# Optimization experiments

Hardware: AMD Instinct MI355X
Metric: run time of the kernel (lower is better)

Reference implementation:

```python
import jax, jax.numpy as jnp
import numpy as np

B, C, H, W = 8, 512, 32, 32
NUM_HEADS, D_K = 8, 64
EPS = 1e-5


def setup_inputs() -> dict:
    key = jax.random.key(0)
    ks = jax.random.split(key, 6)
    s = 1.0 / np.sqrt(C)
    return {
        "x": jax.random.normal(ks[0], (B, C, H, W), dtype=jnp.float32),
        "wq": jax.random.uniform(ks[1], (C, NUM_HEADS * D_K), jnp.float32, -s, s),
        "bq": jnp.zeros((NUM_HEADS * D_K,), jnp.float32),
        "wk": jax.random.uniform(ks[2], (C, NUM_HEADS * D_K), jnp.float32, -s, s),
        "bk": jnp.zeros((NUM_HEADS * D_K,), jnp.float32),
        "wv": jax.random.uniform(ks[3], (C, NUM_HEADS * D_K), jnp.float32, -s, s),
        "bv": jnp.zeros((NUM_HEADS * D_K,), jnp.float32),
        "ln_g": jnp.ones((C,), jnp.float32),
        "ln_b": jnp.zeros((C,), jnp.float32),
        "wo": jax.random.uniform(ks[4], (NUM_HEADS * D_K, C), jnp.float32, -s, s),
        "bo": jnp.zeros((C,), jnp.float32),
    }


def reference(x, wq, bq, wk, bk, wv, bv, ln_g, ln_b, wo, bo):
    b, c, h, w = x.shape
    seq = h * w
    # [B, C, H, W] -> [B, S, C]
    t = x.reshape(b, c, seq).transpose(0, 2, 1)
    residual = t
    # LayerNorm over channel dim
    mu = jnp.mean(t, axis=-1, keepdims=True)
    var = jnp.var(t, axis=-1, keepdims=True)
    tn = (t - mu) * jax.lax.rsqrt(var + EPS) * ln_g + ln_b
    # QKV projections -> [B, S, h, d]
    q = (tn @ wq + bq).reshape(b, seq, NUM_HEADS, D_K)
    k = (tn @ wk + bk).reshape(b, seq, NUM_HEADS, D_K)
    v = (tn @ wv + bv).reshape(b, seq, NUM_HEADS, D_K)
    scores = jnp.einsum("bqhd,bkhd->bhqk", q, k) / np.sqrt(D_K).astype(np.float32)
    attn = jax.nn.softmax(scores, axis=-1)
    out = jnp.einsum("bhqk,bkhd->bqhd", attn, v).reshape(b, seq, NUM_HEADS * D_K)
    out = out @ wo + bo
    return out + residual
```

## Files before the change

kernel.cpp:

```cpp
#include <hip/hip_runtime.h>
#include <hip/hip_bf16.h>
#include <stdint.h>

#define BB 8
#define CC 512
#define SS 1024
#define NH 8
#define DK 64
#define MM (BB*SS)
#define PQ 72

typedef __attribute__((ext_vector_type(8))) short bf16x8;
typedef __attribute__((ext_vector_type(4))) float f32x4;

__device__ inline float b2f(unsigned short u) {
    union { unsigned int i; float f; } x; x.i = ((unsigned int)u) << 16; return x.f;
}
__device__ inline unsigned short f2b(float f) {
    union { float f; unsigned int i; } x; x.f = f;
    unsigned int r = (x.i + 0x7FFFu + ((x.i >> 16) & 1u)) >> 16;
    return (unsigned short)r;
}
__device__ inline unsigned int cvtpk(float lo, float hi) {
    unsigned int r;
    asm("v_cvt_pk_bf16_f32 %0, %1, %2" : "=v"(r) : "v"(lo), "v"(hi));
    return r;
}
__device__ inline f32x4 mfma16(bf16x8 a, bf16x8 b, f32x4 c) {
    return __builtin_amdgcn_mfma_f32_16x16x32_bf16(a, b, c, 0, 0, 0);
}
__device__ __forceinline__ void gload16(const void* g, void* l) {
    __builtin_amdgcn_global_load_lds(
        (const __attribute__((address_space(1))) void*)g,
        (__attribute__((address_space(3))) void*)l, 16, 0, 0);
}

__global__ void __launch_bounds__(256) wtrans_kernel(const float* __restrict__ wq,
                                                     const float* __restrict__ wk,
                                                     const float* __restrict__ wv,
                                                     const float* __restrict__ wo,
                                                     unsigned short* __restrict__ wT) {
    __shared__ float lds[64][65];
    const float* w = (blockIdx.z == 0) ? wq : (blockIdx.z == 1) ? wk : (blockIdx.z == 2) ? wv : wo;
    unsigned short* o = wT + (size_t)blockIdx.z * (512 * 512);
    const int n0 = blockIdx.x * 64, k0 = blockIdx.y * 64;
    const int t = threadIdx.x;
    {
        const int nl = (t & 15) * 4, kr = t >> 4;
#pragma unroll
        for (int i = 0; i < 4; ++i) {
            float4 v = *(const float4*)(w + (size_t)(k0 + kr + i * 16) * 512 + n0 + nl);
            lds[kr + i * 16][nl] = v.x; lds[kr + i * 16][nl + 1] = v.y;
            lds[kr + i * 16][nl + 2] = v.z; lds[kr + i * 16][nl + 3] = v.w;
        }
    }
    __syncthreads();
    {
        const int k8 = (t & 7) * 8, nr = t >> 3;
#pragma unroll
        for (int ii = 0; ii < 2; ++ii) {
            int n = nr + ii * 32;
            unsigned short pk[8];
#pragma unroll
            for (int e = 0; e < 8; ++e) pk[e] = f2b(lds[k8 + e][n]);
            *(uint4*)&o[(size_t)(n0 + n) * 512 + k0 + k8] = *(uint4*)pk;
        }
    }
}

__global__ void __launch_bounds__(256) stats_kernel(const float* __restrict__ x,
                                                    float2* __restrict__ stats) {
    __shared__ float2 red[16][64];
    const int b = blockIdx.y, s0 = blockIdx.x * 64;
    const int sl = (threadIdx.x & 15) * 4, cg = threadIdx.x >> 4;
    float sum[4] = {0.f, 0.f, 0.f, 0.f}, sq[4] = {0.f, 0.f, 0.f, 0.f};
    const float* xp = x + ((size_t)b * 512 + cg * 32) * 1024 + s0 + sl;
#pragma unroll 4
    for (int i = 0; i < 32; ++i) {
        float4 v = *(const float4*)(xp + (size_t)i * 1024);
        sum[0] += v.x; sq[0] += v.x * v.x;
        sum[1] += v.y; sq[1] += v.y * v.y;
        sum[2] += v.z; sq[2] += v.z * v.z;
        sum[3] += v.w; sq[3] += v.w * v.w;
    }
#pragma unroll
    for (int e = 0; e < 4; ++e) red[cg][sl + e] = make_float2(sum[e], sq[e]);
    __syncthreads();
    if (threadIdx.x < 64) {
        float s = 0.f, q = 0.f;
#pragma unroll
        for (int c = 0; c < 16; ++c) { s += red[c][threadIdx.x].x; q += red[c][threadIdx.x].y; }
        float mean = s * (1.f / 512.f);
        float var = q * (1.f / 512.f) - mean * mean;
        stats[b * 1024 + s0 + threadIdx.x] = make_float2(mean, rsqrtf(var + 1e-5f));
    }
}

__global__ void __launch_bounds__(256) xln_kernel(const float* __restrict__ x,
                                                  const float2* __restrict__ stats,
                                                  const float* __restrict__ g,
                                                  const float* __restrict__ bta,
                                                  unsigned short* __restrict__ xt,
                                                  unsigned short* __restrict__ tn) {
    __shared__ float lds[64][65];
    const int s0 = blockIdx.x * 64, c0 = blockIdx.y * 64, b = blockIdx.z;
    const int t = threadIdx.x;
    {
        const int sl = (t & 15) * 4, cr = t >> 4;
#pragma unroll
        for (int i = 0; i < 4; ++i) {
            float4 v = *(const float4*)(x + ((size_t)b * 512 + c0 + cr + i * 16) * 1024 + s0 + sl);
            lds[cr + i * 16][sl] = v.x; lds[cr + i * 16][sl + 1] = v.y;
            lds[cr + i * 16][sl + 2] = v.z; lds[cr + i * 16][sl + 3] = v.w;
        }
    }
    __syncthreads();
    {
        const int c8 = (t & 7) * 8, sr = t >> 3;
        float gg[8], bb[8];
        {
            float4 g0 = *(const float4*)(g + c0 + c8), g1 = *(const float4*)(g + c0 + c8 + 4);
            float4 b0 = *(const float4*)(bta + c0 + c8), b1 = *(const float4*)(bta + c0 + c8 + 4);
            gg[0]=g0.x; gg[1]=g0.y; gg[2]=g0.z; gg[3]=g0.w; gg[4]=g1.x; gg[5]=g1.y; gg[6]=g1.z; gg[7]=g1.w;
            bb[0]=b0.x; bb[1]=b0.y; bb[2]=b0.z; bb[3]=b0.w; bb[4]=b1.x; bb[5]=b1.y; bb[6]=b1.z; bb[7]=b1.w;
        }
#pragma unroll
        for (int ii = 0; ii < 2; ++ii) {
            int s = sr + ii * 32;
            float2 st = stats[b * 1024 + s0 + s];
            unsigned short rawp[8], nrmp[8];
#pragma unroll
            for (int e = 0; e < 8; ++e) {
                float v = lds[c8 + e][s];
                rawp[e] = f2b(v);
                nrmp[e] = f2b((v - st.x) * st.y * gg[e] + bb[e]);
            }
            *(uint4*)&xt[((size_t)b * 1024 + s0 + s) * 512 + c0 + c8] = *(uint4*)rawp;
            *(uint4*)&tn[((size_t)b * 1024 + s0 + s) * 512 + c0 + c8] = *(uint4*)nrmp;
        }
    }
}

__device__ inline void gemm_tile(const unsigned short* __restrict__ A,
                                 const unsigned short* __restrict__ Bt,
                                 int m0, int n0,
                                 unsigned short (*A_lds)[128 * 64],
                                 unsigned short (*B_lds)[128 * 64],
                                 f32x4 acc[4][4]) {
    const int t = threadIdx.x;
    const int lane = t & 63, w = t >> 6;
    const int l15 = lane & 15, l4 = lane >> 4;
    const int wm = (w >> 1) * 64, wn = (w & 1) * 64;
    auto STAGE = [&](int bi, int kt) {
#pragma unroll
        for (int i = 0; i < 4; ++i) {
            int chunk = i * 256 + t;
            int row = chunk >> 3, kc = (chunk & 7) * 8;
            gload16(A + (size_t)(m0 + row) * 512 + kt * 64 + kc, &A_lds[bi][chunk * 8]);
            gload16(Bt + (size_t)(n0 + row) * 512 + kt * 64 + kc, &B_lds[bi][chunk * 8]);
        }
    };
    STAGE(0, 0);
    __syncthreads();
#pragma unroll 1
    for (int kt = 0; kt < 8; ++kt) {
        const int bi = kt & 1;
        if (kt < 7) STAGE(bi ^ 1, kt + 1);
#pragma unroll
        for (int kk = 0; kk < 2; ++kk) {
            bf16x8 af[4], bfr[4];
#pragma unroll
            for (int i = 0; i < 4; ++i)
                af[i] = *(const bf16x8*)&A_lds[bi][(wm + i * 16 + l15) * 64 + kk * 32 + l4 * 8];
#pragma unroll
            for (int j = 0; j < 4; ++j)
                bfr[j] = *(const bf16x8*)&B_lds[bi][(wn + j * 16 + l15) * 64 + kk * 32 + l4 * 8];
#pragma unroll
            for (int i = 0; i < 4; ++i)
#pragma unroll
                for (int j = 0; j < 4; ++j)
                    acc[i][j] = mfma16(af[i], bfr[j], acc[i][j]);
        }
        __syncthreads();
    }
}

__global__ void __launch_bounds__(256) gemm_qkv_kernel(const unsigned short* __restrict__ tn,
                                                       const unsigned short* __restrict__ wT,
                                                       const float* __restrict__ bq,
                                                       const float* __restrict__ bk,
                                                       const float* __restrict__ bv,
                                                       unsigned short* __restrict__ outbase) {
    __shared__ alignas(16) unsigned short A_lds[2][128 * 64];
    __shared__ alignas(16) unsigned short B_lds[2][128 * 64];
    const int z = blockIdx.z;
    const unsigned short* Bt = wT + (size_t)z * (512 * 512);
    const float* bias = (z == 0) ? bq : (z == 1) ? bk : bv;
    const int m0 = blockIdx.x * 128, n0 = blockIdx.y * 128;
    f32x4 acc[4][4];
    const f32x4 z4 = {0.f, 0.f, 0.f, 0.f};
#pragma unroll
    for (int i = 0; i < 4; ++i)
#pragma unroll
        for (int j = 0; j < 4; ++j) acc[i][j] = z4;
    gemm_tile(tn, Bt, m0, n0, A_lds, B_lds, acc);
    const int lane = threadIdx.x & 63, w = threadIdx.x >> 6;
    const int l15 = lane & 15, l4 = lane >> 4;
    const int wm = (w >> 1) * 64, wn = (w & 1) * 64;
    if (z < 2) {
        unsigned short* out = outbase + (size_t)z * MM * 512;
#pragma unroll
        for (int i = 0; i < 4; ++i)
#pragma unroll
            for (int j = 0; j < 4; ++j) {
                int col = n0 + wn + j * 16 + l15;
                float bcol = bias[col];
#pragma unroll
                for (int r = 0; r < 4; ++r) {
                    int row = m0 + wm + i * 16 + l4 * 4 + r;
                    out[(size_t)row * 512 + col] = f2b(acc[i][j][r] + bcol);
                }
            }
    } else {
        unsigned short* vt = outbase + (size_t)2 * MM * 512;
#pragma unroll
        for (int i = 0; i < 4; ++i)
#pragma unroll
            for (int j = 0; j < 4; ++j) {
                int col = n0 + wn + j * 16 + l15;
                float bcol = bias[col];
                int rowb = m0 + wm + i * 16 + l4 * 4;
                int bi = rowb >> 10, s0 = rowb & 1023;
                uint2 pk;
                pk.x = (unsigned int)f2b(acc[i][j][0] + bcol) |
                       ((unsigned int)f2b(acc[i][j][1] + bcol) << 16);
                pk.y = (unsigned int)f2b(acc[i][j][2] + bcol) |
                       ((unsigned int)f2b(acc[i][j][3] + bcol) << 16);
                *(uint2*)&vt[((size_t)bi * 512 + col) * 1024 + s0] = pk;
            }
    }
}

__global__ void __launch_bounds__(512) attn_kernel(const unsigned short* __restrict__ q,
                                                   const unsigned short* __restrict__ k,
                                                   const unsigned short* __restrict__ vt,
                                                   unsigned short* __restrict__ o) {
    __shared__ alignas(16) unsigned short Kl[2][64 * 64];
    __shared__ alignas(16) unsigned short Vl[2][64 * 64];
    __shared__ alignas(16) unsigned short Pl[8][16 * PQ];
    const int pid = blockIdx.x;
    const int g = (pid >> 6) * 8 + (pid & 7);
    const int qt = (pid >> 3) & 7;
    const int b = g >> 3, h = g & 7;
    const int t = threadIdx.x, lane = t & 63, w = t >> 6;
    const int l15 = lane & 15, l4 = lane >> 4;

    const float QSC = 0.125f * 1.44269504f;
    const int qrow = qt * 128 + w * 16 + l15;
    const unsigned short* qp = q + ((size_t)(b * SS + qrow)) * 512 + h * 64;
    bf16x8 qf[2];
#pragma unroll
    for (int kk = 0; kk < 2; ++kk) {
        bf16x8 tmp = *(const bf16x8*)(qp + kk * 32 + l4 * 8);
#pragma unroll
        for (int e = 0; e < 8; ++e)
            tmp[e] = (short)f2b(b2f((unsigned short)tmp[e]) * QSC);
        qf[kk] = tmp;
    }

    const int srow = t >> 3;
    const int scb = ((t & 7) * 16) ^ ((srow & 7) << 4);
    const char* kptr = (const char*)(k + ((size_t)(b * SS) + srow) * 512 + h * 64) + scb;
    const char* vptr = (const char*)(vt + ((size_t)(b * NH + h) * DK + srow) * SS) + scb;

    float m_run = -1e30f, l_run = 0.f;
    f32x4 acc_o[4];
    const f32x4 z4 = {0.f, 0.f, 0.f, 0.f};
#pragma unroll
    for (int j = 0; j < 4; ++j) acc_o[j] = z4;

    gload16(kptr, &Kl[0][t * 8]);
    gload16(vptr, &Vl[0][t * 8]);
    kptr += 64 * 512 * 2;
    vptr += 64 * 2;
    __syncthreads();

#pragma unroll 1
    for (int kt = 0; kt < 16; ++kt) {
        const int bi = kt & 1;
        if (kt < 15) {
            gload16(kptr, &Kl[bi ^ 1][t * 8]);
            gload16(vptr, &Vl[bi ^ 1][t * 8]);
            kptr += 64 * 512 * 2;
            vptr += 64 * 2;
        }

        f32x4 sc[4];
#pragma unroll
        for (int j = 0; j < 4; ++j) sc[j] = z4;
#pragma unroll
        for (int kk = 0; kk < 2; ++kk)
#pragma unroll
            for (int j = 0; j < 4; ++j) {
                int row = j * 16 + l15;
                int cb = (kk * 64 + l4 * 16) ^ ((row & 7) << 4);
                bf16x8 kf = *(const bf16x8*)((const char*)Kl[bi] + row * 128 + cb);
                sc[j] = mfma16(kf, qf[kk], sc[j]);
            }

        float mx = fmaxf(fmaxf(sc[0][0], sc[0][1]), fmaxf(sc[0][2], sc[0][3]));
#pragma unroll
        for (int j = 1; j < 4; ++j)
            mx = fmaxf(mx, fmaxf(fmaxf(sc[j][0], sc[j][1]), fmaxf(sc[j][2], sc[j][3])));
        mx = fmaxf(mx, __shfl_xor(mx, 16));
        mx = fmaxf(mx, __shfl_xor(mx, 32));
        const float mnew = fmaxf(m_run, mx);
        const float scl = exp2f(m_run - mnew);
        m_run = mnew;

        float p[4][4], lsum = 0.f;
#pragma unroll
        for (int j = 0; j < 4; ++j)
#pragma unroll
            for (int r = 0; r < 4; ++r) {
                p[j][r] = exp2f(sc[j][r] - mnew);
                lsum += p[j][r];
            }
        l_run = l_run * scl + lsum;

#pragma unroll
        for (int j = 0; j < 4; ++j) {
            uint2 pk;
            pk.x = cvtpk(p[j][0], p[j][1]);
            pk.y = cvtpk(p[j][2], p[j][3]);
            *(uint2*)&Pl[w][l15 * PQ + j * 16 + l4 * 4] = pk;
        }

        float scl_r[4];
#pragma unroll
        for (int r = 0; r < 4; ++r) scl_r[r] = __shfl(scl, (l4 << 2) | r);
#pragma unroll
        for (int j = 0; j < 4; ++j)
#pragma unroll
            for (int r = 0; r < 4; ++r) acc_o[j][r] *= scl_r[r];

#pragma unroll
        for (int kk = 0; kk < 2; ++kk) {
            bf16x8 pf = *(const bf16x8*)&Pl[w][l15 * PQ + kk * 32 + l4 * 8];
#pragma unroll
            for (int j = 0; j < 4; ++j) {
                int row = j * 16 + l15;
                int cb = (kk * 64 + l4 * 16) ^ ((row & 7) << 4);
                bf16x8 vf = *(const bf16x8*)((const char*)Vl[bi] + row * 128 + cb);
                acc_o[j] = mfma16(pf, vf, acc_o[j]);
            }
        }

        __syncthreads();
    }

    float l_tot = l_run;
    l_tot += __shfl_xor(l_tot, 16);
    l_tot += __shfl_xor(l_tot, 32);
    float l_r[4];
#pragma unroll
    for (int r = 0; r < 4; ++r) l_r[r] = __shfl(l_tot, (l4 << 2) | r);

#pragma unroll
    for (int j = 0; j < 4; ++j)
#pragma unroll
        for (int r = 0; r < 4; ++r) {
            int row = qt * 128 + w * 16 + l4 * 4 + r;
            float val = acc_o[j][r] / l_r[r];
            o[((size_t)(b * SS + row)) * 512 + h * 64 + j * 16 + l15] = f2b(val);
        }
}

__global__ void __launch_bounds__(256) gemm_out_kernel(const unsigned short* __restrict__ ao,
                                                       const unsigned short* __restrict__ woT,
                                                       const float* __restrict__ bo,
                                                       const unsigned short* __restrict__ xt,
                                                       float* __restrict__ out) {
    __shared__ alignas(16) unsigned short A_lds[2][128 * 64];
    __shared__ alignas(16) unsigned short B_lds[2][128 * 64];
    const int m0 = blockIdx.x * 128, n0 = blockIdx.y * 128;
    f32x4 acc[4][4];
    const f32x4 z4 = {0.f, 0.f, 0.f, 0.f};
#pragma unroll
    for (int i = 0; i < 4; ++i)
#pragma unroll
        for (int j = 0; j < 4; ++j) acc[i][j] = z4;
    gemm_tile(ao, woT, m0, n0, A_lds, B_lds, acc);
    const int lane = threadIdx.x & 63, w = threadIdx.x >> 6;
    const int l15 = lane & 15, l4 = lane >> 4;
    const int wm = (w >> 1) * 64, wn = (w & 1) * 64;
#pragma unroll
    for (int i = 0; i < 4; ++i)
#pragma unroll
        for (int j = 0; j < 4; ++j) {
            int col = n0 + wn + j * 16 + l15;
            float bcol = bo[col];
#pragma unroll
            for (int r = 0; r < 4; ++r) {
                int row = m0 + wm + i * 16 + l4 * 4 + r;
                float resid = b2f(xt[(size_t)row * 512 + col]);
                out[(size_t)row * 512 + col] = acc[i][j][r] + bcol + resid;
            }
        }
}

extern "C" void kernel_launch(void* const* d_in, const int* in_sizes, int n_in,
                              void* d_out, int out_size, void* d_ws, size_t ws_size,
                              hipStream_t stream) {
    const float* x   = (const float*)d_in[0];
    const float* wq  = (const float*)d_in[1];
    const float* bq  = (const float*)d_in[2];
    const float* wk  = (const float*)d_in[3];
    const float* bk  = (const float*)d_in[4];
    const float* wv  = (const float*)d_in[5];
    const float* bv  = (const float*)d_in[6];
    const float* lng = (const float*)d_in[7];
    const float* lnb = (const float*)d_in[8];
    const float* wo  = (const float*)d_in[9];
    const float* bo  = (const float*)d_in[10];
    float* out = (float*)d_out;

    unsigned short* ws  = (unsigned short*)d_ws;
    const size_t M1 = (size_t)1024 * 1024;
    unsigned short* tn   = ws;
    unsigned short* qkvb = ws + 4 * M1;
    unsigned short* wT   = ws + 16 * M1;
    unsigned short* xt   = ws + 17 * M1;
    unsigned short* ao   = tn;
    float2* stats = (float2*)qkvb;

    wtrans_kernel<<<dim3(8, 8, 4), 256, 0, stream>>>(wq, wk, wv, wo, wT);
    stats_kernel<<<dim3(16, 8), 256, 0, stream>>>(x, stats);
    xln_kernel<<<dim3(16, 8, 8), 256, 0, stream>>>(x, stats, lng, lnb, xt, tn);
    gemm_qkv_kernel<<<dim3(64, 4, 3), 256, 0, stream>>>(tn, wT, bq, bk, bv, qkvb);
    attn_kernel<<<512, 512, 0, stream>>>(qkvb,
                                         qkvb + (size_t)MM * 512,
                                         qkvb + (size_t)2 * MM * 512,
                                         ao);
    gemm_out_kernel<<<dim3(64, 4), 256, 0, stream>>>(ao, wT + (size_t)3 * 512 * 512, bo, xt, out);
}
```

Baseline: 176.4 us.

## Fuse LayerNorm stats into transpose kernel and vectorize GEMM epilogues via swapped MFMA

```diff
diff --git a/kernel.cpp b/kernel.cpp
--- a/kernel.cpp
+++ b/kernel.cpp
@@ -9,6 +9,7 @@
 #define DK 64
 #define MM (BB*SS)
 #define PQ 72
+#define LNP 40
 
 typedef __attribute__((ext_vector_type(8))) short bf16x8;
 typedef __attribute__((ext_vector_type(4))) float f32x4;
@@ -68,79 +69,71 @@
     }
 }
 
-__global__ void __launch_bounds__(256) stats_kernel(const float* __restrict__ x,
-                                                    float2* __restrict__ stats) {
-    __shared__ float2 red[16][64];
-    const int b = blockIdx.y, s0 = blockIdx.x * 64;
-    const int sl = (threadIdx.x & 15) * 4, cg = threadIdx.x >> 4;
+__global__ void __launch_bounds__(256) xlnf_kernel(const float* __restrict__ x,
+                                                   const float* __restrict__ g,
+                                                   const float* __restrict__ bta,
+                                                   unsigned short* __restrict__ xt,
+                                                   unsigned short* __restrict__ tn) {
+    __shared__ unsigned short raw[512 * LNP];
+    __shared__ float2 red[32][33];
+    __shared__ float2 stf[32];
+    const int b = blockIdx.y, s0 = blockIdx.x * 32;
+    const int t = threadIdx.x;
+    const int sl4 = (t & 7) * 4, crow = t >> 3;
     float sum[4] = {0.f, 0.f, 0.f, 0.f}, sq[4] = {0.f, 0.f, 0.f, 0.f};
-    const float* xp = x + ((size_t)b * 512 + cg * 32) * 1024 + s0 + sl;
-#pragma unroll 4
-    for (int i = 0; i < 32; ++i) {
-        float4 v = *(const float4*)(xp + (size_t)i * 1024);
+#pragma unroll
+    for (int ci = 0; ci < 16; ++ci) {
+        const int c = crow + 32 * ci;
+        float4 v = *(const float4*)(x + ((size_t)b * 512 + c) * 1024 + s0 + sl4);
         sum[0] += v.x; sq[0] += v.x * v.x;
         sum[1] += v.y; sq[1] += v.y * v.y;
         sum[2] += v.z; sq[2] += v.z * v.z;
         sum[3] += v.w; sq[3] += v.w * v.w;
-    }
-#pragma unroll
-    for (int e = 0; e < 4; ++e) red[cg][sl + e] = make_float2(sum[e], sq[e]);
+        const int swz = ((c >> 6) & 3) << 3;
+        uint2 pk;
+        pk.x = (unsigned int)f2b(v.x) | ((unsigned int)f2b(v.y) << 16);
+        pk.y = (unsigned int)f2b(v.z) | ((unsigned int)f2b(v.w) << 16);
+        *(uint2*)&raw[c * LNP + (sl4 ^ swz)] = pk;
+    }
+#pragma unroll
+    for (int e = 0; e < 4; ++e) red[crow][sl4 + e] = make_float2(sum[e], sq[e]);
     __syncthreads();
-    if (threadIdx.x < 64) {
+    if (t < 32) {
         float s = 0.f, q = 0.f;
 #pragma unroll
-        for (int c = 0; c < 16; ++c) { s += red[c][threadIdx.x].x; q += red[c][threadIdx.x].y; }
+        for (int cg = 0; cg < 32; ++cg) { s += red[cg][t].x; q += red[cg][t].y; }
         float mean = s * (1.f / 512.f);
         float var = q * (1.f / 512.f) - mean * mean;
-        stats[b * 1024 + s0 + threadIdx.x] = make_float2(mean, rsqrtf(var + 1e-5f));
-    }
-}
-
-__global__ void __launch_bounds__(256) xln_kernel(const float* __restrict__ x,
-                                                  const float2* __restrict__ stats,
-                                                  const float* __restrict__ g,
-                                                  const float* __restrict__ bta,
-                                                  unsigned short* __restrict__ xt,
-                                                  unsigned short* __restrict__ tn) {
-    __shared__ float lds[64][65];
-    const int s0 = blockIdx.x * 64, c0 = blockIdx.y * 64, b = blockIdx.z;
-    const int t = threadIdx.x;
-    {
-        const int sl = (t & 15) * 4, cr = t >> 4;
-#pragma unroll
-        for (int i = 0; i < 4; ++i) {
-            float4 v = *(const float4*)(x + ((size_t)b * 512 + c0 + cr + i * 16) * 1024 + s0 + sl);
-            lds[cr + i * 16][sl] = v.x; lds[cr + i * 16][sl + 1] = v.y;
-            lds[cr + i * 16][sl + 2] = v.z; lds[cr + i * 16][sl + 3] = v.w;
-        }
+        stf[t] = make_float2(mean, rsqrtf(var + 1e-5f));
     }
     __syncthreads();
     {
-        const int c8 = (t & 7) * 8, sr = t >> 3;
-        float gg[8], bb[8];
-        {
-            float4 g0 = *(const float4*)(g + c0 + c8), g1 = *(const float4*)(g + c0 + c8 + 4);
-            float4 b0 = *(const float4*)(bta + c0 + c8), b1 = *(const float4*)(bta + c0 + c8 + 4);
-            gg[0]=g0.x; gg[1]=g0.y; gg[2]=g0.z; gg[3]=g0.w; gg[4]=g1.x; gg[5]=g1.y; gg[6]=g1.z; gg[7]=g1.w;
-            bb[0]=b0.x; bb[1]=b0.y; bb[2]=b0.z; bb[3]=b0.w; bb[4]=b1.x; bb[5]=b1.y; bb[6]=b1.z; bb[7]=b1.w;
-        }
-#pragma unroll
-        for (int ii = 0; ii < 2; ++ii) {
-            int s = sr + ii * 32;
-            float2 st = stats[b * 1024 + s0 + s];
-            unsigned short rawp[8], nrmp[8];
+        const int srow = t >> 3, cb = (t & 7) * 64;
+        const float2 st = stf[srow];
+        const size_t orow = ((size_t)b * 1024 + s0 + srow) * 512;
+#pragma unroll
+        for (int cc = 0; cc < 64; cc += 8) {
+            const int c0 = cb + cc;
+            unsigned short rv[8], nv[8];
+            const float4 g0 = *(const float4*)(g + c0), g1 = *(const float4*)(g + c0 + 4);
+            const float4 b0 = *(const float4*)(bta + c0), b1 = *(const float4*)(bta + c0 + 4);
+            const float gg[8] = {g0.x, g0.y, g0.z, g0.w, g1.x, g1.y, g1.z, g1.w};
+            const float bb[8] = {b0.x, b0.y, b0.z, b0.w, b1.x, b1.y, b1.z, b1.w};
 #pragma unroll
             for (int e = 0; e < 8; ++e) {
-                float v = lds[c8 + e][s];
-                rawp[e] = f2b(v);
-                nrmp[e] = f2b((v - st.x) * st.y * gg[e] + bb[e]);
-            }
-            *(uint4*)&xt[((size_t)b * 1024 + s0 + s) * 512 + c0 + c8] = *(uint4*)rawp;
-            *(uint4*)&tn[((size_t)b * 1024 + s0 + s) * 512 + c0 + c8] = *(uint4*)nrmp;
-        }
-    }
-}
-
+                const int c = c0 + e;
+                const int swz = ((c >> 6) & 3) << 3;
+                unsigned short u = raw[c * LNP + (srow ^ swz)];
+                rv[e] = u;
+                nv[e] = f2b((b2f(u) - st.x) * st.y * gg[e] + bb[e]);
+            }
+            *(uint4*)&xt[orow + c0] = *(uint4*)rv;
+            *(uint4*)&tn[orow + c0] = *(uint4*)nv;
+        }
+    }
+}
+
+template <bool SWAP>
 __device__ inline void gemm_tile(const unsigned short* __restrict__ A,
                                  const unsigned short* __restrict__ Bt,
                                  int m0, int n0,
@@ -179,7 +172,8 @@
             for (int i = 0; i < 4; ++i)
 #pragma unroll
                 for (int j = 0; j < 4; ++j)
-                    acc[i][j] = mfma16(af[i], bfr[j], acc[i][j]);
+                    acc[i][j] = SWAP ? mfma16(bfr[j], af[i], acc[i][j])
+                                     : mfma16(af[i], bfr[j], acc[i][j]);
         }
         __syncthreads();
     }
@@ -203,25 +197,32 @@
     for (int i = 0; i < 4; ++i)
 #pragma unroll
         for (int j = 0; j < 4; ++j) acc[i][j] = z4;
-    gemm_tile(tn, Bt, m0, n0, A_lds, B_lds, acc);
     const int lane = threadIdx.x & 63, w = threadIdx.x >> 6;
     const int l15 = lane & 15, l4 = lane >> 4;
     const int wm = (w >> 1) * 64, wn = (w & 1) * 64;
     if (z < 2) {
+        gemm_tile<true>(tn, Bt, m0, n0, A_lds, B_lds, acc);
         unsigned short* out = outbase + (size_t)z * MM * 512;
-#pragma unroll
-        for (int i = 0; i < 4; ++i)
+        float4 bias4[4];
+#pragma unroll
+        for (int j = 0; j < 4; ++j)
+            bias4[j] = *(const float4*)(bias + n0 + wn + j * 16 + l4 * 4);
+#pragma unroll
+        for (int i = 0; i < 4; ++i) {
+            const size_t row = (size_t)(m0 + wm + i * 16 + l15);
 #pragma unroll
             for (int j = 0; j < 4; ++j) {
-                int col = n0 + wn + j * 16 + l15;
-                float bcol = bias[col];
-#pragma unroll
-                for (int r = 0; r < 4; ++r) {
-                    int row = m0 + wm + i * 16 + l4 * 4 + r;
-                    out[(size_t)row * 512 + col] = f2b(acc[i][j][r] + bcol);
-                }
-            }
+                const int nc = n0 + wn + j * 16 + l4 * 4;
+                uint2 pk;
+                pk.x = (unsigned int)f2b(acc[i][j][0] + bias4[j].x) |
+                       ((unsigned int)f2b(acc[i][j][1] + bias4[j].y) << 16);
+                pk.y = (unsigned int)f2b(acc[i][j][2] + bias4[j].z) |
+                       ((unsigned int)f2b(acc[i][j][3] + bias4[j].w) << 16);
+                *(uint2*)&out[row * 512 + nc] = pk;
+            }
+        }
     } else {
+        gemm_tile<false>(tn, Bt, m0, n0, A_lds, B_lds, acc);
         unsigned short* vt = outbase + (size_t)2 * MM * 512;
 #pragma unroll
         for (int i = 0; i < 4; ++i)
@@ -390,23 +391,29 @@
     for (int i = 0; i < 4; ++i)
 #pragma unroll
         for (int j = 0; j < 4; ++j) acc[i][j] = z4;
-    gemm_tile(ao, woT, m0, n0, A_lds, B_lds, acc);
+    gemm_tile<true>(ao, woT, m0, n0, A_lds, B_lds, acc);
     const int lane = threadIdx.x & 63, w = threadIdx.x >> 6;
     const int l15 = lane & 15, l4 = lane >> 4;
     const int wm = (w >> 1) * 64, wn = (w & 1) * 64;
-#pragma unroll
-    for (int i = 0; i < 4; ++i)
+    float4 bias4[4];
+#pragma unroll
+    for (int j = 0; j < 4; ++j)
+        bias4[j] = *(const float4*)(bo + n0 + wn + j * 16 + l4 * 4);
+#pragma unroll
+    for (int i = 0; i < 4; ++i) {
+        const size_t row = (size_t)(m0 + wm + i * 16 + l15);
 #pragma unroll
         for (int j = 0; j < 4; ++j) {
-            int col = n0 + wn + j * 16 + l15;
-            float bcol = bo[col];
-#pragma unroll
-            for (int r = 0; r < 4; ++r) {
-                int row = m0 + wm + i * 16 + l4 * 4 + r;
-                float resid = b2f(xt[(size_t)row * 512 + col]);
-                out[(size_t)row * 512 + col] = acc[i][j][r] + bcol + resid;
-            }
-        }
+            const int nc = n0 + wn + j * 16 + l4 * 4;
+            uint2 rv = *(const uint2*)&xt[row * 512 + nc];
+            float4 o4;
+            o4.x = acc[i][j][0] + bias4[j].x + b2f((unsigned short)(rv.x & 0xffff));
+            o4.y = acc[i][j][1] + bias4[j].y + b2f((unsigned short)(rv.x >> 16));
+            o4.z = acc[i][j][2] + bias4[j].z + b2f((unsigned short)(rv.y & 0xffff));
+            o4.w = acc[i][j][3] + bias4[j].w + b2f((unsigned short)(rv.y >> 16));
+            *(float4*)&out[row * 512 + nc] = o4;
+        }
+    }
 }
 
 extern "C" void kernel_launch(void* const* d_in, const int* in_sizes, int n_in,
@@ -432,11 +439,9 @@
     unsigned short* wT   = ws + 16 * M1;
     unsigned short* xt   = ws + 17 * M1;
     unsigned short* ao   = tn;
-    float2* stats = (float2*)qkvb;
 
     wtrans_kernel<<<dim3(8, 8, 4), 256, 0, stream>>>(wq, wk, wv, wo, wT);
-    stats_kernel<<<dim3(16, 8), 256, 0, stream>>>(x, stats);
-    xln_kernel<<<dim3(16, 8, 8), 256, 0, stream>>>(x, stats, lng, lnb, xt, tn);
+    xlnf_kernel<<<dim3(32, 8), 256, 0, stream>>>(x, lng, lnb, xt, tn);
     gemm_qkv_kernel<<<dim3(64, 4, 3), 256, 0, stream>>>(tn, wT, bq, bk, bv, qkvb);
     attn_kernel<<<512, 512, 0, stream>>>(qkvb,
                                          qkvb + (size_t)MM * 512,
```

Result: slower. 181.4 us (+2.9%).
